# Kernel tuning notes

Measured on AMD Instinct MI355X. Metric: run time of the kernel, lower is better.

Reference implementation:

```python
import jax, jax.numpy as jnp
import numpy as np

EPS = 1e-5

def _layernorm(x, g, b):
    mu = jnp.mean(x, axis=-1, keepdims=True)
    var = jnp.mean(jnp.square(x - mu), axis=-1, keepdims=True)
    return (x - mu) * jax.lax.rsqrt(var + EPS) * g + b

def _silu(x):
    return x * jax.nn.sigmoid(x)

def _xavier(key, shape):
    fan_out, fan_in = shape
    limit = np.sqrt(6.0 / (fan_in + fan_out))
    return jax.random.uniform(key, shape, jnp.float32, -limit, limit)

def setup_inputs() -> dict:
    key = jax.random.key(0)
    ks = jax.random.split(key, 4)
    B = 2097152
    return {
        'x': jax.random.normal(ks[0], (B, 24), jnp.float32),
        'w1': _xavier(ks[1], (64, 24)), 'b1': jnp.zeros((64,), jnp.float32),
        'g1': jnp.ones((64,), jnp.float32), 'be1': jnp.zeros((64,), jnp.float32),
        'w2': _xavier(ks[2], (64, 64)), 'b2': jnp.zeros((64,), jnp.float32),
        'g2': jnp.ones((64,), jnp.float32), 'be2': jnp.zeros((64,), jnp.float32),
        'w3': _xavier(ks[3], (7, 64)), 'b3': jnp.zeros((7,), jnp.float32),
        'g3': jnp.ones((7,), jnp.float32), 'be3': jnp.zeros((7,), jnp.float32),
    }

def reference(x, w1, b1, g1, be1, w2, b2, g2, be2, w3, b3, g3, be3):
    h = _silu(_layernorm(x @ w1.T + b1, g1, be1))      # [B, 64]
    h = _silu(_layernorm(h @ w2.T + b2, g2, be2))      # [B, 64]
    h = _layernorm(h @ w3.T + b3, g3, be3)             # [B, 7]
    return jax.nn.softmax(h, axis=-1)
```

## Files before the change

### kernel.cpp

```cpp
#include <hip/hip_runtime.h>
#include <math.h>

#define BLOCK 256
#define WPB 4
#define NBLOCKS 2048

typedef float  f32x4 __attribute__((ext_vector_type(4)));
typedef float  f32x2 __attribute__((ext_vector_type(2)));
typedef short  short8 __attribute__((ext_vector_type(8)));
typedef unsigned int u32;
typedef u32 u32x4 __attribute__((ext_vector_type(4)));
typedef u32 u32x2 __attribute__((ext_vector_type(2)));

static __device__ __forceinline__ f32x4 mfma16(short8 a, short8 b, f32x4 c) {
    return __builtin_amdgcn_mfma_f32_16x16x32_bf16(a, b, c, 0, 0, 0);
}

static __device__ __forceinline__ f32x4 zero4() { f32x4 z = {0.f, 0.f, 0.f, 0.f}; return z; }

static __device__ __forceinline__ u32 cvt_pk(float lo, float hi) {
    u32 r;
    asm("v_cvt_pk_bf16_f32 %0, %1, %2" : "=v"(r) : "v"(lo), "v"(hi));
    return r;
}
static __device__ __forceinline__ float unpk_lo(u32 p) { return __builtin_bit_cast(float, p << 16); }
static __device__ __forceinline__ float unpk_hi(u32 p) { return __builtin_bit_cast(float, p & 0xffff0000u); }

static __device__ __forceinline__ short8 mk_frag(u32 a, u32 b, u32 c, u32 d) {
    u32x4 t = {a, b, c, d};
    return __builtin_bit_cast(short8, t);
}

struct Frag2 { short8 hi, lo; };

static __device__ __forceinline__ Frag2 split8(f32x4 a, f32x4 b) {
    u32 h0 = cvt_pk(a[0], a[1]), h1 = cvt_pk(a[2], a[3]);
    u32 h2 = cvt_pk(b[0], b[1]), h3 = cvt_pk(b[2], b[3]);
    u32 l0 = cvt_pk(a[0] - unpk_lo(h0), a[1] - unpk_hi(h0));
    u32 l1 = cvt_pk(a[2] - unpk_lo(h1), a[3] - unpk_hi(h1));
    u32 l2 = cvt_pk(b[0] - unpk_lo(h2), b[1] - unpk_hi(h2));
    u32 l3 = cvt_pk(b[2] - unpk_lo(h3), b[3] - unpk_hi(h3));
    Frag2 r; r.hi = mk_frag(h0, h1, h2, h3); r.lo = mk_frag(l0, l1, l2, l3);
    return r;
}

static __device__ __forceinline__ void split4(f32x4 v, u32x2& hi, u32x2& lo) {
    u32 h0 = cvt_pk(v[0], v[1]), h1 = cvt_pk(v[2], v[3]);
    u32 l0 = cvt_pk(v[0] - unpk_lo(h0), v[1] - unpk_hi(h0));
    u32 l1 = cvt_pk(v[2] - unpk_lo(h1), v[3] - unpk_hi(h1));
    hi = u32x2{h0, h1}; lo = u32x2{l0, l1};
}

static __device__ __forceinline__ Frag2 wfrag(const float* p) {
    return split8(*(const f32x4*)p, *(const f32x4*)(p + 4));
}

static __device__ __forceinline__ float red4(float v) {
    v += __shfl_xor(v, 16);
    v += __shfl_xor(v, 32);
    return v;
}
static __device__ __forceinline__ float redmax4(float v) {
    v = fmaxf(v, __shfl_xor(v, 16));
    v = fmaxf(v, __shfl_xor(v, 32));
    return v;
}

struct TState {
    f32x4 xa, xb;
    f32x4 d[4];
    short8 bhHi[2], bhLo[2];
    f32x4 d3;
};

static __device__ __forceinline__ void ph_l1(TState& t, const Frag2& bx, const Frag2* w1f) {
#pragma unroll
    for (int mt = 0; mt < 4; ++mt) {
        f32x4 d = mfma16(w1f[mt].hi, bx.hi, zero4());
        d = mfma16(w1f[mt].hi, bx.lo, d);
        d = mfma16(w1f[mt].lo, bx.hi, d);
        t.d[mt] = d;
    }
}

static __device__ __forceinline__ void ph_l2(TState& t, const Frag2 (*w2f)[2]) {
#pragma unroll
    for (int mt = 0; mt < 4; ++mt) {
        f32x4 d = mfma16(w2f[mt][0].hi, t.bhHi[0], zero4());
        d = mfma16(w2f[mt][0].hi, t.bhLo[0], d);
        d = mfma16(w2f[mt][0].lo, t.bhHi[0], d);
        d = mfma16(w2f[mt][1].hi, t.bhHi[1], d);
        d = mfma16(w2f[mt][1].hi, t.bhLo[1], d);
        d = mfma16(w2f[mt][1].lo, t.bhHi[1], d);
        t.d[mt] = d;
    }
}

static __device__ __forceinline__ void ph_l3(TState& t, const Frag2* w3f) {
    f32x4 a = mfma16(w3f[0].hi, t.bhHi[0], zero4());
    a = mfma16(w3f[0].hi, t.bhLo[0], a);
    a = mfma16(w3f[0].lo, t.bhHi[0], a);
    f32x4 b = mfma16(w3f[1].hi, t.bhHi[1], zero4());
    b = mfma16(w3f[1].hi, t.bhLo[1], b);
    b = mfma16(w3f[1].lo, t.bhHi[1], b);
#pragma unroll
    for (int r = 0; r < 4; ++r) t.d3[r] = a[r] + b[r];
}

template<int PB, int PG, int PBE>
static __device__ __forceinline__ void ph_ln_silu(TState& t, const float* sP, int q) {
    float s = 0.f, s2 = 0.f;
#pragma unroll
    for (int mt = 0; mt < 4; ++mt) {
        if (PB >= 0) {
            const f32x4 bv = *(const f32x4*)(sP + PB + mt * 16 + q * 4);
#pragma unroll
            for (int r = 0; r < 4; ++r) t.d[mt][r] += bv[r];
        }
#pragma unroll
        for (int r = 0; r < 4; ++r) { float v = t.d[mt][r]; s += v; s2 = fmaf(v, v, s2); }
    }
    s = red4(s); s2 = red4(s2);
    const float mu = s * (1.f / 64.f);
    const float var = s2 * (1.f / 64.f) - mu * mu;
    const float inv = __builtin_amdgcn_rsqf(var + 1e-5f);
    const float cns = -mu * inv;
#pragma unroll
    for (int mt = 0; mt < 4; ++mt) {
        const f32x4 gv  = *(const f32x4*)(sP + PG  + mt * 16 + q * 4);
        const f32x4 bev = *(const f32x4*)(sP + PBE + mt * 16 + q * 4);
#pragma unroll
        for (int r = 0; r < 4; ++r) {
            float tt = fmaf(t.d[mt][r], inv, cns);
            float v  = fmaf(tt, gv[r], bev[r]);
            t.d[mt][r] = v * __builtin_amdgcn_rcpf(1.f + __expf(-v));
        }
    }
}

static __device__ __forceinline__ void ph_stage(TState& t, unsigned char* sHi, unsigned char* sLo,
                                                u32 crow, u32 ch, int q) {
#pragma unroll
    for (int mt = 0; mt < 4; ++mt) {
        u32x2 hi, lo;
        split4(t.d[mt], hi, lo);
        u32 off = crow + ((((u32)(mt * 2 + (q >> 1))) ^ ch) << 4) + (u32)((q & 1) * 8);
        *(u32x2*)(sHi + off) = hi;
        *(u32x2*)(sLo + off) = lo;
    }
#pragma unroll
    for (int kk = 0; kk < 2; ++kk) {
        u32 roff = crow + ((((u32)(kk * 4 + q)) ^ ch) << 4);
        t.bhHi[kk] = *(const short8*)(sHi + roff);
        t.bhLo[kk] = *(const short8*)(sLo + roff);
    }
}

static __device__ __forceinline__ void ph_out(TState& t, const float* sP, int q, int c, int lane,
                                              unsigned char* ob, float* out, int tile, bool valid,
                                              int oc0, int of0, int oc1, int of1) {
    const f32x4 b3v  = *(const f32x4*)(sP + 384 + q * 4);
    const f32x4 g3v  = *(const f32x4*)(sP + 400 + q * 4);
    const f32x4 be3v = *(const f32x4*)(sP + 416 + q * 4);
    f32x4 d3 = t.d3;
    float s = 0.f, s2 = 0.f;
#pragma unroll
    for (int r = 0; r < 4; ++r) {
        float v = d3[r] + b3v[r];
        d3[r] = v;
        const bool ok = (q * 4 + r) < 7;
        if (ok) { s += v; s2 = fmaf(v, v, s2); }
    }
    s = red4(s); s2 = red4(s2);
    const float mu = s * (1.f / 7.f);
    const float var = s2 * (1.f / 7.f) - mu * mu;
    const float inv = __builtin_amdgcn_rsqf(var + 1e-5f);
    const float cns = -mu * inv;

    float z[4]; float mx = -1e30f;
#pragma unroll
    for (int r = 0; r < 4; ++r) {
        z[r] = fmaf(fmaf(d3[r], inv, cns), g3v[r], be3v[r]);
        const bool ok = (q * 4 + r) < 7;
        if (ok) mx = fmaxf(mx, z[r]);
    }
    mx = redmax4(mx);
    float es = 0.f; float e[4];
#pragma unroll
    for (int r = 0; r < 4; ++r) {
        const bool ok = (q * 4 + r) < 7;
        e[r] = ok ? __expf(z[r] - mx) : 0.f;
        es += e[r];
    }
    es = red4(es);
    const float rs = __builtin_amdgcn_rcpf(es);

    if (q == 0) {
        f32x4 v = {e[0] * rs, e[1] * rs, e[2] * rs, e[3] * rs};
        *(f32x4*)(ob + c * 48) = v;
    } else if (q == 1) {
        f32x2 v = {e[0] * rs, e[1] * rs};
        *(f32x2*)(ob + c * 48 + 16) = v;
        *(float*)(ob + c * 48 + 24) = e[2] * rs;
    }
    if (valid) {
        float* outp = out + (size_t)tile * 112;
        outp[lane] = *(const float*)(ob + oc0 * 48 + of0 * 4);
        if (lane < 48) outp[64 + lane] = *(const float*)(ob + oc1 * 48 + of1 * 4);
    }
}

__global__ __launch_bounds__(BLOCK, 2) void mlp_mfma2_kernel(
    const float* __restrict__ x,
    const float* __restrict__ w1, const float* __restrict__ b1,
    const float* __restrict__ g1, const float* __restrict__ be1,
    const float* __restrict__ w2, const float* __restrict__ b2,
    const float* __restrict__ g2, const float* __restrict__ be2,
    const float* __restrict__ w3, const float* __restrict__ b3,
    const float* __restrict__ g3, const float* __restrict__ be3,
    float* __restrict__ out, int ntiles)
{
    __shared__ __align__(16) unsigned char smem[WPB * (2 * 4096 + 2 * 768)];
    __shared__ __align__(16) float sP[6 * 64 + 3 * 16];

    const int tid = threadIdx.x;
    const int lane = tid & 63;
    const int wib  = tid >> 6;
    const int c = lane & 15;
    const int q = lane >> 4;

    if (tid < 64) {
        sP[        tid] = b1[tid];  sP[ 64 + tid] = g1[tid];  sP[128 + tid] = be1[tid];
        sP[192 + tid] = b2[tid];    sP[256 + tid] = g2[tid];  sP[320 + tid] = be2[tid];
    }
    if (tid < 16) {
        const bool ok = tid < 7;
        sP[384 + tid] = ok ? b3[tid]  : 0.f;
        sP[400 + tid] = ok ? g3[tid]  : 0.f;
        sP[416 + tid] = ok ? be3[tid] : 0.f;
    }

    unsigned char* wb   = smem + wib * (2 * 4096 + 2 * 768);
    unsigned char* sHiA = wb;
    unsigned char* sLoA = wb + 2048;
    unsigned char* sHiB = wb + 4096;
    unsigned char* sLoB = wb + 6144;
    unsigned char* obA  = wb + 8192;
    unsigned char* obB  = wb + 8960;

    const u32 crow = (u32)c * 128u;
    const u32 ch   = (u32)(c & 7);

    Frag2 w1f[4];
#pragma unroll
    for (int mt = 0; mt < 4; ++mt) {
        if (q < 3) {
            w1f[mt] = wfrag(w1 + (mt * 16 + c) * 24 + q * 8);
        } else {
            float s = b1[mt * 16 + c];
            f32x4 a = {s, 0.f, 0.f, 0.f};
            w1f[mt] = split8(a, zero4());
        }
    }
    Frag2 w2f[4][2];
#pragma unroll
    for (int mt = 0; mt < 4; ++mt)
#pragma unroll
        for (int kk = 0; kk < 2; ++kk)
            w2f[mt][kk] = wfrag(w2 + (mt * 16 + c) * 64 + kk * 32 + q * 8);
    Frag2 w3f[2];
#pragma unroll
    for (int kk = 0; kk < 2; ++kk) {
        if (c < 7) w3f[kk] = wfrag(w3 + c * 64 + kk * 32 + q * 8);
        else       { w3f[kk].hi = mk_frag(0,0,0,0); w3f[kk].lo = mk_frag(0,0,0,0); }
    }

    __syncthreads();

    const int oc0 = lane / 7, of0 = lane - oc0 * 7;
    const int i1 = lane + 64;
    const int oc1 = i1 / 7, of1 = i1 - oc1 * 7;

    const int wid = blockIdx.x * WPB + wib;
    const int ts  = gridDim.x * WPB;

    TState A, B;
    A.xa = zero4(); A.xb = zero4(); B.xa = zero4(); B.xb = zero4();
    {
        const int t0 = wid, t1 = wid + ts;
        if (t0 < ntiles && q < 3) {
            const float* xp = x + ((size_t)t0 * 16 + c) * 24 + q * 8;
            A.xa = *(const f32x4*)xp; A.xb = *(const f32x4*)(xp + 4);
        }
        if (t1 < ntiles && q < 3) {
            const float* xp = x + ((size_t)t1 * 16 + c) * 24 + q * 8;
            B.xa = *(const f32x4*)xp; B.xb = *(const f32x4*)(xp + 4);
        }
        if (q == 3) { A.xa[0] = 1.0f; B.xa[0] = 1.0f; }
    }

    for (int tile = wid; tile < ntiles; tile += 2 * ts) {
        asm volatile("" ::: "memory");

        const int tB = tile + ts;
        const bool vB = tB < ntiles;

        Frag2 bxA = split8(A.xa, A.xb);
        Frag2 bxB = split8(B.xa, B.xb);

        {
            const int tA2 = tile + 2 * ts, tB2 = tile + 3 * ts;
            if (tA2 < ntiles && q < 3) {
                const float* xp = x + ((size_t)tA2 * 16 + c) * 24 + q * 8;
                A.xa = *(const f32x4*)xp; A.xb = *(const f32x4*)(xp + 4);
            }
            if (tB2 < ntiles && q < 3) {
                const float* xp = x + ((size_t)tB2 * 16 + c) * 24 + q * 8;
                B.xa = *(const f32x4*)xp; B.xb = *(const f32x4*)(xp + 4);
            }
        }

        ph_l1(A, bxA, w1f);                 ph_l1(B, bxB, w1f);
        ph_ln_silu<-1, 64, 128>(A, sP, q);  ph_ln_silu<-1, 64, 128>(B, sP, q);
        ph_stage(A, sHiA, sLoA, crow, ch, q); ph_stage(B, sHiB, sLoB, crow, ch, q);
        ph_l2(A, w2f);                      ph_l2(B, w2f);
        ph_ln_silu<192, 256, 320>(A, sP, q); ph_ln_silu<192, 256, 320>(B, sP, q);
        ph_stage(A, sHiA, sLoA, crow, ch, q); ph_stage(B, sHiB, sLoB, crow, ch, q);
        ph_l3(A, w3f);                      ph_l3(B, w3f);
        ph_out(A, sP, q, c, lane, obA, out, tile, true, oc0, of0, oc1, of1);
        ph_out(B, sP, q, c, lane, obB, out, tB,   vB,   oc0, of0, oc1, of1);
    }
}

extern "C" void kernel_launch(void* const* d_in, const int* in_sizes, int n_in,
                              void* d_out, int out_size, void* d_ws, size_t ws_size,
                              hipStream_t stream) {
    const float* x   = (const float*)d_in[0];
    const float* w1  = (const float*)d_in[1];
    const float* b1  = (const float*)d_in[2];
    const float* g1  = (const float*)d_in[3];
    const float* be1 = (const float*)d_in[4];
    const float* w2  = (const float*)d_in[5];
    const float* b2  = (const float*)d_in[6];
    const float* g2  = (const float*)d_in[7];
    const float* be2 = (const float*)d_in[8];
    const float* w3  = (const float*)d_in[9];
    const float* b3  = (const float*)d_in[10];
    const float* g3  = (const float*)d_in[11];
    const float* be3 = (const float*)d_in[12];
    float* out = (float*)d_out;

    const int B = in_sizes[0] / 24;
    const int ntiles = B / 16;
    hipLaunchKernelGGL(mlp_mfma2_kernel, dim3(NBLOCKS), dim3(BLOCK), 0, stream,
                       x, w1, b1, g1, be1, w2, b2, g2, be2, w3, b3, g3, be3,
                       out, ntiles);
}
```

Measured before the change: 200.7 us.

## Move W2 fragments from registers to swizzled shared memory, raise occupancy to 3

The second-layer weight fragments (hi/lo bf16 splits) no longer live in per-thread registers. They are built once per block into a shared, XOR-swizzled LDS buffer and reloaded per tile, and one set of loads now serves both in-flight tiles A and B. The output staging buffers are aliased onto the activation staging area to cut LDS, and launch bounds go from 2 to 3 waves per SIMD to allow more resident waves. This trades VGPR pressure for extra LDS reads in the layer-2 loop, and it relies on the aliasing being safe with respect to ph_stage and ph_out ordering.

```diff
diff --git a/kernel.cpp b/kernel.cpp
--- a/kernel.cpp
+++ b/kernel.cpp
@@ -83,16 +83,31 @@
     }
 }
 
-static __device__ __forceinline__ void ph_l2(TState& t, const Frag2 (*w2f)[2]) {
-#pragma unroll
-    for (int mt = 0; mt < 4; ++mt) {
-        f32x4 d = mfma16(w2f[mt][0].hi, t.bhHi[0], zero4());
-        d = mfma16(w2f[mt][0].hi, t.bhLo[0], d);
-        d = mfma16(w2f[mt][0].lo, t.bhHi[0], d);
-        d = mfma16(w2f[mt][1].hi, t.bhHi[1], d);
-        d = mfma16(w2f[mt][1].hi, t.bhLo[1], d);
-        d = mfma16(w2f[mt][1].lo, t.bhHi[1], d);
-        t.d[mt] = d;
+static __device__ __forceinline__ void ph_l2_pair(TState& A, TState& B,
+        const unsigned char* sW2h, const unsigned char* sW2l, u32 crow, u32 ch, int q) {
+    const u32 r0 = crow + ((((u32)q) ^ ch) << 4);
+    const u32 r1 = crow + ((((u32)(4 + q)) ^ ch) << 4);
+#pragma unroll
+    for (int mt = 0; mt < 4; ++mt) {
+        const u32 mo = (u32)mt * 2048u;
+        short8 h0 = *(const short8*)(sW2h + mo + r0);
+        short8 h1 = *(const short8*)(sW2h + mo + r1);
+        short8 l0 = *(const short8*)(sW2l + mo + r0);
+        short8 l1 = *(const short8*)(sW2l + mo + r1);
+        f32x4 d = mfma16(h0, A.bhHi[0], zero4());
+        d = mfma16(h0, A.bhLo[0], d);
+        d = mfma16(l0, A.bhHi[0], d);
+        d = mfma16(h1, A.bhHi[1], d);
+        d = mfma16(h1, A.bhLo[1], d);
+        d = mfma16(l1, A.bhHi[1], d);
+        A.d[mt] = d;
+        f32x4 e = mfma16(h0, B.bhHi[0], zero4());
+        e = mfma16(h0, B.bhLo[0], e);
+        e = mfma16(l0, B.bhHi[0], e);
+        e = mfma16(h1, B.bhHi[1], e);
+        e = mfma16(h1, B.bhLo[1], e);
+        e = mfma16(l1, B.bhHi[1], e);
+        B.d[mt] = e;
     }
 }
 
@@ -210,7 +225,7 @@
     }
 }
 
-__global__ __launch_bounds__(BLOCK, 2) void mlp_mfma2_kernel(
+__global__ __launch_bounds__(BLOCK, 3) void mlp_mfma3_kernel(
     const float* __restrict__ x,
     const float* __restrict__ w1, const float* __restrict__ b1,
     const float* __restrict__ g1, const float* __restrict__ be1,
@@ -220,7 +235,7 @@
     const float* __restrict__ g3, const float* __restrict__ be3,
     float* __restrict__ out, int ntiles)
 {
-    __shared__ __align__(16) unsigned char smem[WPB * (2 * 4096 + 2 * 768)];
+    __shared__ __align__(16) unsigned char smem[WPB * 8192 + 16384];
     __shared__ __align__(16) float sP[6 * 64 + 3 * 16];
 
     const int tid = threadIdx.x;
@@ -229,6 +244,23 @@
     const int c = lane & 15;
     const int q = lane >> 4;
 
+    unsigned char* wb   = smem + wib * 8192;
+    unsigned char* sHiA = wb;
+    unsigned char* sLoA = wb + 2048;
+    unsigned char* sHiB = wb + 4096;
+    unsigned char* sLoB = wb + 6144;
+    unsigned char* obA  = sHiA;
+    unsigned char* obB  = sHiB;
+    unsigned char* sW2h = smem + WPB * 8192;
+    unsigned char* sW2l = sW2h + 8192;
+
+    for (int i = tid; i < 512; i += BLOCK) {
+        const int row = i >> 3, cb = i & 7;
+        Frag2 f = wfrag(w2 + row * 64 + cb * 8);
+        const u32 off = (u32)row * 128u + (u32)((cb ^ (row & 7)) << 4);
+        *(short8*)(sW2h + off) = f.hi;
+        *(short8*)(sW2l + off) = f.lo;
+    }
     if (tid < 64) {
         sP[        tid] = b1[tid];  sP[ 64 + tid] = g1[tid];  sP[128 + tid] = be1[tid];
         sP[192 + tid] = b2[tid];    sP[256 + tid] = g2[tid];  sP[320 + tid] = be2[tid];
@@ -239,14 +271,6 @@
         sP[400 + tid] = ok ? g3[tid]  : 0.f;
         sP[416 + tid] = ok ? be3[tid] : 0.f;
     }
-
-    unsigned char* wb   = smem + wib * (2 * 4096 + 2 * 768);
-    unsigned char* sHiA = wb;
-    unsigned char* sLoA = wb + 2048;
-    unsigned char* sHiB = wb + 4096;
-    unsigned char* sLoB = wb + 6144;
-    unsigned char* obA  = wb + 8192;
-    unsigned char* obB  = wb + 8960;
 
     const u32 crow = (u32)c * 128u;
     const u32 ch   = (u32)(c & 7);
@@ -262,12 +286,6 @@
             w1f[mt] = split8(a, zero4());
         }
     }
-    Frag2 w2f[4][2];
-#pragma unroll
-    for (int mt = 0; mt < 4; ++mt)
-#pragma unroll
-        for (int kk = 0; kk < 2; ++kk)
-            w2f[mt][kk] = wfrag(w2 + (mt * 16 + c) * 64 + kk * 32 + q * 8);
     Frag2 w3f[2];
 #pragma unroll
     for (int kk = 0; kk < 2; ++kk) {
@@ -323,7 +341,7 @@
         ph_l1(A, bxA, w1f);                 ph_l1(B, bxB, w1f);
         ph_ln_silu<-1, 64, 128>(A, sP, q);  ph_ln_silu<-1, 64, 128>(B, sP, q);
         ph_stage(A, sHiA, sLoA, crow, ch, q); ph_stage(B, sHiB, sLoB, crow, ch, q);
-        ph_l2(A, w2f);                      ph_l2(B, w2f);
+        ph_l2_pair(A, B, sW2h, sW2l, crow, ch, q);
         ph_ln_silu<192, 256, 320>(A, sP, q); ph_ln_silu<192, 256, 320>(B, sP, q);
         ph_stage(A, sHiA, sLoA, crow, ch, q); ph_stage(B, sHiB, sLoB, crow, ch, q);
         ph_l3(A, w3f);                      ph_l3(B, w3f);
@@ -352,7 +370,7 @@
 
     const int B = in_sizes[0] / 24;
     const int ntiles = B / 16;
-    hipLaunchKernelGGL(mlp_mfma2_kernel, dim3(NBLOCKS), dim3(BLOCK), 0, stream,
+    hipLaunchKernelGGL(mlp_mfma3_kernel, dim3(NBLOCKS), dim3(BLOCK), 0, stream,
                        x, w1, b1, g1, be1, w2, b2, g2, be2, w3, b3, g3, be3,
                        out, ntiles);
 }
```

Result: slower. 224.5 us (+11.9%).
